# Kernel tuning notes

Measured on AMD Instinct MI355X. Metric: run time of the kernel, lower is better.

## Reference

```python
import jax, jax.numpy as jnp
import numpy as np

NEG = -1e18


def _split_heads(x, h):
    # [B, L, D] -> [B, H, L, D/H]
    b, l, d = x.shape
    return x.reshape(b, l, h, d // h).transpose(0, 2, 1, 3)


def _merge_heads(x):
    # [B, H, L, Dh] -> [B, L, H*Dh]
    b, h, l, dh = x.shape
    return x.transpose(0, 2, 1, 3).reshape(b, l, h * dh)


def _sparse(att, dp_map):
    # att: [B, H, L] per-token scores; dp_map: [B, 2, L] (row, col) tree indices.
    # scatter att[b,h,t] -> S[b, h, dp_map[b,0,t], dp_map[b,1,t]], then symmetrize.
    B, H, L = att.shape
    bi = jnp.arange(B)[:, None, None]          # [B,1,1]
    hi = jnp.arange(H)[None, :, None]          # [1,H,1]
    p0 = dp_map[:, 0, :][:, None, :]           # [B,1,L]
    p1 = dp_map[:, 1, :][:, None, :]           # [B,1,L]
    s = jnp.zeros((B, H, L, L), att.dtype)
    s = s.at[bi, hi, p0, p1].set(att)          # matches torch index_put_ (overwrite)
    return s + jnp.swapaxes(s, 2, 3)


def _reverse(values, dp_map):
    # r[b, j] = values[b, dp_map[b,0,j]] for j >= 1; r[b,0] = 0
    idx = dp_map[:, 0, :]                      # [B, L]
    r = jnp.take_along_axis(values, idx[:, :, None], axis=1)
    return r.at[:, 0, :].set(0.0)


def setup_inputs() -> dict:
    key = jax.random.key(0)
    ks = jax.random.split(key, 16)
    B, L, D, R, H = 16, 384, 768, 768, 12
    inp = {
        "queries":   jax.random.normal(ks[0], (B, L, D), jnp.float32),
        "keys":      jax.random.normal(ks[1], (B, L, D), jnp.float32),
        "values":    jax.random.normal(ks[2], (B, L, D), jnp.float32),
        "relations": jax.random.normal(ks[3], (B, L, R), jnp.float32),
        "dp_map":    jax.random.randint(ks[4], (B, 2, L), 0, L, jnp.int32),
        "mask":      jax.random.bernoulli(ks[5], 0.1, (B, L, L)),
        "rel_mask":  jax.random.bernoulli(ks[6], 0.1, (B, L, 1)),
        "Wq":  jax.random.normal(ks[7],  (D, D), jnp.float32) * 0.02,
        "Wk":  jax.random.normal(ks[8],  (D, D), jnp.float32) * 0.02,
        "Wv":  jax.random.normal(ks[9],  (D, D), jnp.float32) * 0.02,
        "Wo":  jax.random.normal(ks[10], (D, D), jnp.float32) * 0.02,
        "Wge": jax.random.normal(ks[11], (D, R), jnp.float32) * 0.02,
        "Wgr": jax.random.normal(ks[12], (R, R), jnp.float32) * 0.02,
        "Vr":  jax.random.normal(ks[13], (R, 1), jnp.float32) * 0.02,
        "Vg":  jax.random.normal(ks[14], (R, 1), jnp.float32) * 0.02,
    }
    return inp


def reference(queries, keys, values, relations, dp_map, mask, rel_mask,
              Wq, Wk, Wv, Wo, Wge, Wgr, Vr, Vg):
    H = 12
    R = Vg.shape[0]
    Dk = Wq.shape[1]
    scale = (Dk // H) ** -0.5

    # config.is_reverse = True path
    hv = jnp.where(rel_mask, 0.0, _reverse(values, dp_map))       # [B,L,D]
    rel = jnp.where(rel_mask, 0.0, relations)                     # [B,L,R]

    # semantic gated mechanism
    rv_h = _split_heads(rel @ Wgr, H)                             # [B,H,L,R/H]
    hs_h = _split_heads(hv @ Wge, H)
    Vg_h = Vg.reshape(H, R // H, 1)
    g = jnp.tanh(jnp.einsum('bhld,hdo->bhlo', hs_h + rv_h, Vg_h))[..., 0]
    gated = _sparse(g, dp_map)                                    # [B,H,L,L]

    q = _split_heads(queries @ Wq, H) * scale
    k = _split_heads(keys @ Wk, H)
    v = _split_heads(values @ Wv, H)
    rel_h = _split_heads(rel, H)
    Vr_h = Vr.reshape(H, R // H, 1)

    self_logits = jnp.einsum('bhqd,bhkd->bhqk', q, k)             # [B,H,L,L]
    rel_logits = _sparse(jnp.einsum('bhld,hdo->bhlo', rel_h, Vr_h)[..., 0], dp_map)

    m = mask[:, None]                                             # [B,1,L,L]
    self_logits = jnp.where(m, NEG, self_logits)
    rel_logits = jnp.where(m, NEG, rel_logits)

    attention_weights = self_logits.sum(axis=1) / H               # [B,L,L]
    sw = jax.nn.softmax(self_logits, axis=-1)
    rw = jax.nn.softmax(rel_logits, axis=-1)
    w = (1.0 - gated) * sw + gated * rw                           # dropout p=0

    ctx = jnp.einsum('bhqk,bhkd->bhqd', w, v)
    out = _merge_heads(ctx) @ Wo
    return out, attention_weights
```

## Files before the change

kernel.cpp:

```cpp
#include <hip/hip_runtime.h>
#include <math.h>

#define Bn 16
#define Lq 384
#define Hn 12
#define Dm 768
#define DH 64
#define QT2 16
#define NEGV (-1e18f)
#define SPADU 404
#define ECAP 32

typedef __attribute__((ext_vector_type(4))) float f32x4;
typedef __attribute__((ext_vector_type(8))) __bf16 bf16x8;
typedef __attribute__((ext_vector_type(4))) __bf16 bf16x4;
typedef unsigned short ushort_t;
typedef unsigned int uint_t;
typedef unsigned long long ull_t;

__device__ __forceinline__ ushort_t f2b(float f) {
  return __builtin_bit_cast(ushort_t, (__bf16)f);
}
__device__ __forceinline__ float b2f(ushort_t u) {
  return __uint_as_float(((unsigned int)u) << 16);
}
__device__ __forceinline__ bf16x8 cvt8(float4 a, float4 b) {
  bf16x8 r;
  r[0] = (__bf16)a.x; r[1] = (__bf16)a.y; r[2] = (__bf16)a.z; r[3] = (__bf16)a.w;
  r[4] = (__bf16)b.x; r[5] = (__bf16)b.y; r[6] = (__bf16)b.z; r[7] = (__bf16)b.w;
  return r;
}

__global__ __launch_bounds__(256) void k_prep(
    const float* __restrict__ Wge, const float* __restrict__ Wgr,
    const float* __restrict__ Vg,
    float* __restrict__ Age, float* __restrict__ Agr,
    const float* __restrict__ W0, const float* __restrict__ W1,
    const float* __restrict__ W2, const float* __restrict__ W3,
    ushort_t* __restrict__ T0, ushort_t* __restrict__ T1,
    ushort_t* __restrict__ T2, ushort_t* __restrict__ T3,
    const int* __restrict__ dp, int* __restrict__ win,
    const int* __restrict__ mask, ull_t* __restrict__ mbits)
{
  __shared__ float vg[DH];
  __shared__ float t[32][33];
  int blk = blockIdx.x;
  if (blk < 24) {
    int which = blk / Hn;
    int h = blk % Hn;
    const float* Wsrc = which ? Wgr : Wge;
    float* dst = which ? Agr : Age;
    if (threadIdx.x < DH) vg[threadIdx.x] = Vg[h*DH + threadIdx.x];
    __syncthreads();
    for (int d = threadIdx.x; d < Dm; d += 256) {
      const float* wrow = Wsrc + (size_t)d*Dm + h*DH;
      float s = 0.f;
      #pragma unroll 8
      for (int j = 0; j < DH; ++j) s = fmaf(wrow[j], vg[j], s);
      dst[h*Dm + d] = s;
    }
  } else if (blk < 24 + 2304) {
    int b2 = blk - 24;
    int z = b2 / 576, rem = b2 % 576;
    const float* W = (z == 0) ? W0 : (z == 1) ? W1 : (z == 2) ? W2 : W3;
    ushort_t* WT = (z == 0) ? T0 : (z == 1) ? T1 : (z == 2) ? T2 : T3;
    int k0 = (rem / 24)*32, n0 = (rem % 24)*32;
    int tx = threadIdx.x & 31, ty = threadIdx.x >> 5;
    #pragma unroll
    for (int r = 0; r < 4; ++r)
      t[ty + r*8][tx] = W[(size_t)(k0 + ty + r*8)*Dm + n0 + tx];
    __syncthreads();
    #pragma unroll
    for (int r = 0; r < 4; ++r)
      WT[(size_t)(n0 + ty + r*8)*Dm + k0 + tx] = f2b(t[tx][ty + r*8]);
  } else if (blk < 2352) {
    int i = (blk - 2328)*256 + threadIdx.x;
    int b = i / Lq, l = i % Lq;
    int p0 = dp[(size_t)(b*2+0)*Lq + l];
    int p1 = dp[(size_t)(b*2+1)*Lq + l];
    atomicMax(&win[(size_t)b*Lq*Lq + (size_t)p0*Lq + p1], l);
  } else {
    int rr = blk - 2352;
    int lane = threadIdx.x & 63, wave = threadIdx.x >> 6;
    int gi = rr*4 + wave;
    const int* mrow = mask + (size_t)gi*Lq;
    ull_t w0 = __ballot(mrow[lane]        != 0);
    ull_t w1 = __ballot(mrow[lane + 64]   != 0);
    ull_t w2 = __ballot(mrow[lane + 128]  != 0);
    ull_t w3 = __ballot(mrow[lane + 192]  != 0);
    ull_t w4 = __ballot(mrow[lane + 256]  != 0);
    ull_t w5 = __ballot(mrow[lane + 320]  != 0);
    if (lane == 0) {
      ull_t* out = mbits + (size_t)gi*6;
      out[0] = w0; out[1] = w1; out[2] = w2;
      out[3] = w3; out[4] = w4; out[5] = w5;
    }
  }
}

__global__ __launch_bounds__(256) void k_collect(
    const int* __restrict__ win, uint_t* __restrict__ ent,
    int* __restrict__ rowcnt)
{
  __shared__ int tB[32][33];
  int b = blockIdx.z;
  int i0 = blockIdx.x*32, j0 = blockIdx.y*32;
  const int* wb = win + (size_t)b*Lq*Lq;
  int tx = threadIdx.x & 31, ty = threadIdx.x >> 5;
  #pragma unroll
  for (int rr = 0; rr < 4; ++rr) {
    int r = ty + rr*8;
    tB[r][tx] = wb[(size_t)(j0+r)*Lq + i0 + tx];
  }
  __syncthreads();
  #pragma unroll
  for (int rr = 0; rr < 4; ++rr) {
    int ti = ty + rr*8;
    int i = i0 + ti, j = j0 + tx;
    int l1 = wb[(size_t)i*Lq + j];
    int l2 = tB[tx][ti];
    if (l1 >= 0 || l2 >= 0) {
      int slot = atomicAdd(&rowcnt[(size_t)b*Lq + i], 1);
      if (slot < ECAP)
        ent[((size_t)b*Lq + i)*ECAP + slot] =
            (uint_t)j | ((uint_t)(l1 + 1) << 9) | ((uint_t)(l2 + 1) << 19);
    }
  }
}

__global__ __launch_bounds__(256) void k_grlog(
    const float* __restrict__ values, const float* __restrict__ relations,
    const int* __restrict__ dp, const int* __restrict__ rel_mask,
    const float* __restrict__ Age, const float* __restrict__ Agr,
    const float* __restrict__ Vr,
    float* __restrict__ g, float* __restrict__ rlog)
{
  int blk = blockIdx.x;
  int b = blk / (Lq/4), l0 = (blk % (Lq/4))*4;
  int tid = threadIdx.x, lane = tid & 63, wave = tid >> 6;
  __shared__ float relrow[4][Dm], hvrow[4][Dm];
  #pragma unroll
  for (int rr = 0; rr < 4; ++rr) {
    int l = l0 + rr;
    int rm = rel_mask[(size_t)b*Lq + l];
    int idx = dp[(size_t)(b*2)*Lq + l];
    const float* vrow = values + ((size_t)b*Lq + idx)*Dm;
    const float* rrow = relations + ((size_t)b*Lq + l)*Dm;
    for (int d = tid; d < Dm; d += 256) {
      relrow[rr][d] = rm ? 0.f : rrow[d];
      hvrow[rr][d]  = (rm || l == 0) ? 0.f : vrow[d];
    }
  }
  __syncthreads();
  int l = l0 + wave;
  for (int h = 0; h < Hn; ++h) {
    float p = 0.f;
    #pragma unroll
    for (int k = 0; k < Dm/64; ++k) {
      int d = lane + 64*k;
      p = fmaf(hvrow[wave][d], Age[h*Dm + d],
          fmaf(relrow[wave][d], Agr[h*Dm + d], p));
    }
    #pragma unroll
    for (int o = 32; o > 0; o >>= 1) p += __shfl_xor(p, o);
    if (lane == 0) g[((size_t)b*Hn + h)*Lq + l] = tanhf(p);
  }
  if (lane < Hn) {
    float s = 0.f;
    #pragma unroll 8
    for (int j = 0; j < DH; ++j)
      s = fmaf(relrow[wave][lane*DH + j], Vr[lane*DH + j], s);
    rlog[((size_t)b*Hn + lane)*Lq + l] = s;
  }
}

__global__ __launch_bounds__(256) void k_mmqkv(
    const float* __restrict__ Xq, const float* __restrict__ Xk,
    const float* __restrict__ Xv,
    const ushort_t* __restrict__ WqT, const ushort_t* __restrict__ WkT,
    const ushort_t* __restrict__ WvT,
    ushort_t* __restrict__ qbf, ushort_t* __restrict__ kbf,
    ushort_t* __restrict__ vTbf)
{
  __shared__ ushort_t As[64*64];
  __shared__ ushort_t Bs[128*64];

  int z = blockIdx.z;
  const float* A     = (z == 0) ? Xq : (z == 1) ? Xk : Xv;
  const ushort_t* BT = (z == 0) ? WqT : (z == 1) ? WkT : WvT;

  int bm = blockIdx.x;
  int bn = blockIdx.y;
  int m0 = bm*64, n0 = bn*128;

  int t = threadIdx.x;
  int wave = t >> 6, lane = t & 63;
  int wr = wave >> 1, wc = wave & 1;
  int lrow = lane & 15, lkg = lane >> 4;
  int sr = t >> 3, sc8 = t & 7;

  f32x4 acc[2][4];
  #pragma unroll
  for (int i = 0; i < 2; ++i)
    #pragma unroll
    for (int j = 0; j < 4; ++j) acc[i][j] = (f32x4)(0.f);

  for (int k0 = 0; k0 < Dm; k0 += 64) {
    __syncthreads();
    #pragma unroll
    for (int i = 0; i < 2; ++i) {
      int row = sr + i*32;
      const float* ap = A + (size_t)(m0 + row)*Dm + k0 + sc8*8;
      float4 f0 = *(const float4*)ap;
      float4 f1 = *(const float4*)(ap + 4);
      *(bf16x8*)&As[row*64 + (sc8 ^ (row & 7))*8] = cvt8(f0, f1);
    }
    #pragma unroll
    for (int i = 0; i < 4; ++i) {
      int row = sr + i*32;
      uint4 vb = *(const uint4*)(BT + (size_t)(n0 + row)*Dm + k0 + sc8*8);
      *(uint4*)&Bs[row*64 + (sc8 ^ (row & 7))*8] = vb;
    }
    __syncthreads();
    #pragma unroll
    for (int kk = 0; kk < 2; ++kk) {
      bf16x8 aF[2], bF[4];
      int chunk = kk*4 + lkg;
      #pragma unroll
      for (int mi = 0; mi < 2; ++mi) {
        int arow = wr*32 + mi*16 + lrow;
        aF[mi] = *(const bf16x8*)&As[arow*64 + ((chunk ^ (arow & 7)) << 3)];
      }
      #pragma unroll
      for (int ni = 0; ni < 4; ++ni) {
        int brow = wc*64 + ni*16 + lrow;
        bF[ni] = *(const bf16x8*)&Bs[brow*64 + ((chunk ^ (brow & 7)) << 3)];
      }
      #pragma unroll
      for (int mi = 0; mi < 2; ++mi)
        #pragma unroll
        for (int ni = 0; ni < 4; ++ni)
          acc[mi][ni] = __builtin_amdgcn_mfma_f32_16x16x32_bf16(
              aF[mi], bF[ni], acc[mi][ni], 0, 0, 0);
    }
  }

  float alpha = (z == 0) ? 0.125f : 1.f;
  #pragma unroll
  for (int mi = 0; mi < 2; ++mi) {
    #pragma unroll
    for (int ni = 0; ni < 4; ++ni) {
      f32x4 a = acc[mi][ni];
      int rit = wr*32 + mi*16 + 4*lkg;
      int cit = wc*64 + ni*16 + lrow;
      int gcol = n0 + cit;
      if (z < 2) {
        ushort_t* Cb = z ? kbf : qbf;
        int grow = m0 + rit;
        #pragma unroll
        for (int r = 0; r < 4; ++r)
          Cb[(size_t)(grow + r)*Dm + gcol] = f2b(a[r]*alpha);
      } else {
        int b = bm/6;
        int rl = (bm%6)*64 + rit;
        ushort4 u;
        u.x = f2b(a[0]); u.y = f2b(a[1]); u.z = f2b(a[2]); u.w = f2b(a[3]);
        *(ushort4*)&vTbf[((size_t)b*Dm + gcol)*Lq + rl] = u;
      }
    }
  }
}

template<int MODE>
__global__ __launch_bounds__(256) void k_mm64(
    const ushort_t* __restrict__ A, const ushort_t* __restrict__ BT,
    float* __restrict__ Cf, const int* __restrict__ mask, float alpha)
{
  const int K = Dm;
  __shared__ ushort_t As[64*64];
  __shared__ ushort_t Bs[128*64];

  int bm = blockIdx.x, bn = blockIdx.y, b = blockIdx.z;
  const ushort_t* Ab = (MODE == 3) ? A  + (size_t)b*Lq*Dm : A;
  const ushort_t* Bb = (MODE == 3) ? BT + (size_t)b*Lq*Dm : BT;
  int m0 = bm*64, n0 = bn*128;

  int t = threadIdx.x;
  int wave = t >> 6, lane = t & 63;
  int wr = wave >> 1, wc = wave & 1;
  int lrow = lane & 15, lkg = lane >> 4;

  f32x4 acc[2][4];
  #pragma unroll
  for (int i = 0; i < 2; ++i)
    #pragma unroll
    for (int j = 0; j < 4; ++j) acc[i][j] = (f32x4)(0.f);

  int sr = t >> 3, sc8 = t & 7;
  for (int k0 = 0; k0 < K; k0 += 64) {
    __syncthreads();
    #pragma unroll
    for (int i = 0; i < 2; ++i) {
      int row = sr + i*32;
      uint4 va = *(const uint4*)(Ab + (size_t)(m0 + row)*K + k0 + sc8*8);
      int slot = sc8 ^ (row & 7);
      *(uint4*)&As[row*64 + slot*8] = va;
    }
    #pragma unroll
    for (int i = 0; i < 4; ++i) {
      int row = sr + i*32;
      uint4 vb = *(const uint4*)(Bb + (size_t)(n0 + row)*K + k0 + sc8*8);
      int slot = sc8 ^ (row & 7);
      *(uint4*)&Bs[row*64 + slot*8] = vb;
    }
    __syncthreads();
    #pragma unroll
    for (int kk = 0; kk < 2; ++kk) {
      bf16x8 aF[2], bF[4];
      int chunk = kk*4 + lkg;
      #pragma unroll
      for (int mi = 0; mi < 2; ++mi) {
        int arow = wr*32 + mi*16 + lrow;
        aF[mi] = *(const bf16x8*)&As[arow*64 + ((chunk ^ (arow & 7)) << 3)];
      }
      #pragma unroll
      for (int ni = 0; ni < 4; ++ni) {
        int brow = wc*64 + ni*16 + lrow;
        bF[ni] = *(const bf16x8*)&Bs[brow*64 + ((chunk ^ (brow & 7)) << 3)];
      }
      #pragma unroll
      for (int mi = 0; mi < 2; ++mi)
        #pragma unroll
        for (int ni = 0; ni < 4; ++ni)
          acc[mi][ni] = __builtin_amdgcn_mfma_f32_16x16x32_bf16(
              aF[mi], bF[ni], acc[mi][ni], 0, 0, 0);
    }
  }

  #pragma unroll
  for (int mi = 0; mi < 2; ++mi) {
    #pragma unroll
    for (int ni = 0; ni < 4; ++ni) {
      f32x4 a = acc[mi][ni];
      int rit = wr*32 + mi*16 + 4*lkg;
      int cit = wc*64 + ni*16 + lrow;
      if (MODE == 0) {
        int grow = m0 + rit, gcol = n0 + cit;
        #pragma unroll
        for (int r = 0; r < 4; ++r)
          Cf[(size_t)(grow + r)*Dm + gcol] = a[r]*alpha;
      } else {
        int rl = m0 + rit, cl = n0 + cit;
        const int* mb2 = mask + (size_t)b*Lq*Lq;
        float* awb = Cf + (size_t)b*Lq*Lq;
        #pragma unroll
        for (int r = 0; r < 4; ++r) {
          int m = mb2[(size_t)(rl + r)*Lq + cl];
          awb[(size_t)(rl + r)*Lq + cl] = m ? NEGV : a[r]*alpha;
        }
      }
    }
  }
}

__global__ __launch_bounds__(256, 8) void k_attn3(
    const ushort_t* __restrict__ qbf, const ushort_t* __restrict__ kbf,
    const ushort_t* __restrict__ vT,
    const ull_t* __restrict__ mbits, const int* __restrict__ rowcnt,
    const uint_t* __restrict__ ent,
    const float* __restrict__ g, const float* __restrict__ rlog,
    ushort_t* __restrict__ ctxbf)
{
  __shared__ ushort_t S16[QT2][SPADU];
  __shared__ ull_t mb[QT2][6];
  __shared__ float2 rg2[Lq + 1];
  __shared__ uint_t entS[QT2*ECAP];
  __shared__ int cntS[QT2];
  __shared__ float pp[QT2][4];
  __shared__ float sinvS[QT2];

  int bid = blockIdx.x;
  int h  = bid % Hn;
  int qt = (bid / Hn) % (Lq/QT2);
  int b  = bid / (Hn * (Lq/QT2));
  int q0 = qt * QT2;
  int tid = threadIdx.x, lane = tid & 63, wave = tid >> 6;
  int lrow = lane & 15, lkg = lane >> 4;

  const float* gh = g    + ((size_t)b*Hn + h)*Lq;
  const float* rh = rlog + ((size_t)b*Hn + h)*Lq;

  if (tid < QT2*6) {
    int r = tid / 6, u = tid % 6;
    mb[r][u] = mbits[((size_t)b*Lq + q0 + r)*6 + u];
  }
  if (tid == 0) { rg2[0].x = 0.f; rg2[0].y = 0.f; }
  for (int e = tid; e < Lq; e += 256) {
    float2 v2; v2.x = rh[e]; v2.y = gh[e];
    rg2[e + 1] = v2;
  }
  #pragma unroll
  for (int e = tid; e < QT2*ECAP; e += 256)
    entS[e] = ent[((size_t)b*Lq + q0)*ECAP + e];
  if (tid < QT2) {
    int c = rowcnt[(size_t)b*Lq + q0 + tid];
    cntS[tid] = c > ECAP ? ECAP : c;
  }
  __syncthreads();

  {
    const ushort_t* qb = qbf + ((size_t)b*Lq + q0 + lrow)*Dm + h*DH + lkg*8;
    bf16x8 aF0 = *(const bf16x8*)(qb);
    bf16x8 aF1 = *(const bf16x8*)(qb + 32);
    int col0 = wave*96;
    int w0 = col0 >> 6;
    ull_t m0[4], m1[4];
    #pragma unroll
    for (int r = 0; r < 4; ++r) {
      m0[r] = mb[4*lkg + r][w0];
      m1[r] = mb[4*lkg + r][w0 + 1];
    }
    float ps[4] = {0.f, 0.f, 0.f, 0.f};
    const ushort_t* kb = kbf + ((size_t)b*Lq + col0 + lrow)*Dm + h*DH + lkg*8;
    #pragma unroll
    for (int tt = 0; tt < 6; ++tt) {
      int col = col0 + tt*16 + lrow;
      bf16x8 bF0 = *(const bf16x8*)(kb);
      bf16x8 bF1 = *(const bf16x8*)(kb + 32);
      kb += 16*Dm;
      f32x4 z = (f32x4)(0.f);
      z = __builtin_amdgcn_mfma_f32_16x16x32_bf16(aF0, bF0, z, 0, 0, 0);
      z = __builtin_amdgcn_mfma_f32_16x16x32_bf16(aF1, bF1, z, 0, 0, 0);
      bool hi = ((col0 + tt*16) >> 6) != w0;
      int sh = col & 63;
      #pragma unroll
      for (int r = 0; r < 4; ++r) {
        ull_t mw = hi ? m1[r] : m0[r];
        bool mk = (mw >> sh) & 1ull;
        float e = mk ? 0.f : __expf(z[r]);
        ps[r] += e;
        S16[4*lkg + r][col] = f2b(e);
      }
    }
    #pragma unroll
    for (int off = 1; off < 16; off <<= 1)
      #pragma unroll
      for (int r = 0; r < 4; ++r) ps[r] += __shfl_xor(ps[r], off);
    if (lrow == 0) {
      #pragma unroll
      for (int r = 0; r < 4; ++r) pp[4*lkg + r][wave] = ps[r];
    }
  }
  __syncthreads();

  if (tid < QT2) {
    int row = tid;
    float ssum = pp[row][0] + pp[row][1] + pp[row][2] + pp[row][3];
    float si = 1.f / ssum;
    sinvS[row] = si;
    int nun = 384;
    #pragma unroll
    for (int u = 0; u < 6; ++u) nun -= (int)__popcll(mb[row][u]);
    int cnt = cntS[row];
    const uint_t* erow = &entS[row*ECAP];
    float rext = 0.f;
    for (int e = 0; e < cnt; ++e) {
      uint_t en = erow[e];
      int j = en & 511;
      if ((mb[row][j >> 6] >> (j & 63)) & 1ull) continue;
      float rel = rg2[(en >> 9) & 1023].x + rg2[en >> 19].x;
      rext += __expf(rel) - 1.f;
    }
    float sr = ssum / ((float)nun + rext);
    for (int e = 0; e < cnt; ++e) {
      uint_t en = erow[e];
      int j = en & 511;
      if ((mb[row][j >> 6] >> (j & 63)) & 1ull) continue;
      float2 a = rg2[(en >> 9) & 1023];
      float2 c = rg2[en >> 19];
      float er = __expf(a.x + c.x);
      float gvv = a.y + c.y;
      float ev = b2f(S16[row][j]);
      S16[row][j] = f2b((1.f - gvv)*ev + gvv*er*sr);
    }
  }
  __syncthreads();

  {
    int dcol = h*DH + wave*16 + lrow;
    const ushort_t* vb = vT + ((size_t)b*Dm + dcol)*Lq + lkg*8;
    const ushort_t* prow = &S16[lrow][0];
    f32x4 o = (f32x4)(0.f);
    #pragma unroll
    for (int ks = 0; ks < 12; ++ks) {
      bf16x4 lo = *(const bf16x4*)(prow + ks*32 + lkg*8);
      bf16x4 hi = *(const bf16x4*)(prow + ks*32 + lkg*8 + 4);
      bf16x8 pa = __builtin_shufflevector(lo, hi, 0,1,2,3,4,5,6,7);
      bf16x8 bv = *(const bf16x8*)(vb + ks*32);
      o = __builtin_amdgcn_mfma_f32_16x16x32_bf16(pa, bv, o, 0, 0, 0);
    }
    #pragma unroll
    for (int r = 0; r < 4; ++r) {
      float si = sinvS[4*lkg + r];
      ctxbf[((size_t)b*Lq + q0 + 4*lkg + r)*Dm + dcol] = f2b(o[r]*si);
    }
  }
}

extern "C" void kernel_launch(void* const* d_in, const int* in_sizes, int n_in,
                              void* d_out, int out_size, void* d_ws, size_t ws_size,
                              hipStream_t stream) {
  const float* queries   = (const float*)d_in[0];
  const float* keys      = (const float*)d_in[1];
  const float* values    = (const float*)d_in[2];
  const float* relations = (const float*)d_in[3];
  const int*   dp_map    = (const int*)d_in[4];
  const int*   mask      = (const int*)d_in[5];
  const int*   rel_mask  = (const int*)d_in[6];
  const float* Wq  = (const float*)d_in[7];
  const float* Wk  = (const float*)d_in[8];
  const float* Wv  = (const float*)d_in[9];
  const float* Wo  = (const float*)d_in[10];
  const float* Wge = (const float*)d_in[11];
  const float* Wgr = (const float*)d_in[12];
  const float* Vr  = (const float*)d_in[13];
  const float* Vg  = (const float*)d_in[14];

  float* ws = (float*)d_ws;
  const size_t SZ   = (size_t)Bn*Lq*Dm;
  const size_t WINS = (size_t)Bn*Lq*Lq;
  const size_t GSZ  = (size_t)Bn*Hn*Lq;
  const size_t ROWS = (size_t)Bn*Lq;

  int*   win  = (int*)ws;
  float* g    = ws + WINS;
  float* rlog = g + GSZ;
  float* Age  = rlog + GSZ;
  float* Agr  = Age + (size_t)Hn*Dm;
  ull_t* mbits = (ull_t*)(Agr + (size_t)Hn*Dm);
  int*   rowcnt = (int*)(mbits + ROWS*6);
  uint_t* ent  = (uint_t*)(rowcnt + ROWS);
  ushort_t* p0 = (ushort_t*)(ent + ROWS*ECAP);
  ushort_t* qbf  = p0;
  ushort_t* kbf  = p0 + SZ;
  ushort_t* vTbf = p0 + 2*SZ;
  ushort_t* ctxbf= p0 + 3*SZ;
  ushort_t* WqT  = p0 + 4*SZ;
  ushort_t* WkT  = WqT + (size_t)Dm*Dm;
  ushort_t* WvT  = WkT + (size_t)Dm*Dm;
  ushort_t* WoT  = WvT + (size_t)Dm*Dm;

  float* outp = (float*)d_out;
  float* awp  = outp + SZ;

  hipMemsetAsync(win, 0xFF, WINS*sizeof(int), stream);
  hipMemsetAsync(rowcnt, 0, ROWS*sizeof(int), stream);
  k_prep<<<3888, 256, 0, stream>>>(Wge, Wgr, Vg, Age, Agr,
                                   Wq, Wk, Wv, Wo, WqT, WkT, WvT, WoT,
                                   dp_map, win, mask, mbits);
  k_grlog<<<Bn*Lq/4, 256, 0, stream>>>(values, relations, dp_map, rel_mask,
                                       Age, Agr, Vr, g, rlog);
  k_mmqkv<<<dim3(96, 6, 3), 256, 0, stream>>>(queries, keys, values,
                                              WqT, WkT, WvT, qbf, kbf, vTbf);
  k_collect<<<dim3(12, 12, Bn), 256, 0, stream>>>(win, ent, rowcnt);
  k_mm64<3><<<dim3(6, 3, Bn), 256, 0, stream>>>(qbf, kbf, awp, mask, 1.f/12.f);
  k_attn3<<<Bn*(Lq/QT2)*Hn, 256, 0, stream>>>(qbf, kbf, vTbf, mbits, rowcnt,
                                              ent, g, rlog, ctxbf);
  k_mm64<0><<<dim3(96, 6, 1), 256, 0, stream>>>(ctxbf, WoT, outp, nullptr, 1.f);
}
```

Baseline: 195.0 us.

## Merge independent stage kernels into two block-dispatched megakernels

Independent kernels (gate/relation logits, QKV projection, entry collection) are merged into one launch. Attention-weight GEMM and attention are merged into a second launch, each dispatching by block index into device functions that share a fixed shared-memory buffer. This cuts launch count and lets independent work from different stages overlap on the GPU. In exchange, every block reserves the largest shared-memory footprint, and the attention kernel loses its occupancy launch-bound hint, which may reduce residency for attention blocks.

```diff
diff --git a/kernel.cpp b/kernel.cpp
--- a/kernel.cpp
+++ b/kernel.cpp
@@ -30,6 +30,8 @@
   r[4] = (__bf16)b.x; r[5] = (__bf16)b.y; r[6] = (__bf16)b.z; r[7] = (__bf16)b.w;
   return r;
 }
+
+#define SMEM_BYTES 24576
 
 __global__ __launch_bounds__(256) void k_prep(
     const float* __restrict__ Wge, const float* __restrict__ Wgr,
@@ -98,47 +100,17 @@
   }
 }
 
-__global__ __launch_bounds__(256) void k_collect(
-    const int* __restrict__ win, uint_t* __restrict__ ent,
-    int* __restrict__ rowcnt)
-{
-  __shared__ int tB[32][33];
-  int b = blockIdx.z;
-  int i0 = blockIdx.x*32, j0 = blockIdx.y*32;
-  const int* wb = win + (size_t)b*Lq*Lq;
-  int tx = threadIdx.x & 31, ty = threadIdx.x >> 5;
-  #pragma unroll
-  for (int rr = 0; rr < 4; ++rr) {
-    int r = ty + rr*8;
-    tB[r][tx] = wb[(size_t)(j0+r)*Lq + i0 + tx];
-  }
-  __syncthreads();
-  #pragma unroll
-  for (int rr = 0; rr < 4; ++rr) {
-    int ti = ty + rr*8;
-    int i = i0 + ti, j = j0 + tx;
-    int l1 = wb[(size_t)i*Lq + j];
-    int l2 = tB[tx][ti];
-    if (l1 >= 0 || l2 >= 0) {
-      int slot = atomicAdd(&rowcnt[(size_t)b*Lq + i], 1);
-      if (slot < ECAP)
-        ent[((size_t)b*Lq + i)*ECAP + slot] =
-            (uint_t)j | ((uint_t)(l1 + 1) << 9) | ((uint_t)(l2 + 1) << 19);
-    }
-  }
-}
-
-__global__ __launch_bounds__(256) void k_grlog(
+
+__device__ void dev_grlog(char* sm, int blk,
     const float* __restrict__ values, const float* __restrict__ relations,
     const int* __restrict__ dp, const int* __restrict__ rel_mask,
     const float* __restrict__ Age, const float* __restrict__ Agr,
-    const float* __restrict__ Vr,
-    float* __restrict__ g, float* __restrict__ rlog)
-{
-  int blk = blockIdx.x;
+    const float* __restrict__ Vr, float* __restrict__ g, float* __restrict__ rlog)
+{
+  float (*relrow)[Dm] = (float(*)[Dm])sm;
+  float (*hvrow)[Dm]  = (float(*)[Dm])(sm + 4*Dm*sizeof(float));
   int b = blk / (Lq/4), l0 = (blk % (Lq/4))*4;
   int tid = threadIdx.x, lane = tid & 63, wave = tid >> 6;
-  __shared__ float relrow[4][Dm], hvrow[4][Dm];
   #pragma unroll
   for (int rr = 0; rr < 4; ++rr) {
     int l = l0 + rr;
@@ -174,7 +146,7 @@
   }
 }
 
-__global__ __launch_bounds__(256) void k_mmqkv(
+__device__ void dev_mmqkv(char* sm, int bm, int bn, int z,
     const float* __restrict__ Xq, const float* __restrict__ Xk,
     const float* __restrict__ Xv,
     const ushort_t* __restrict__ WqT, const ushort_t* __restrict__ WkT,
@@ -182,17 +154,11 @@
     ushort_t* __restrict__ qbf, ushort_t* __restrict__ kbf,
     ushort_t* __restrict__ vTbf)
 {
-  __shared__ ushort_t As[64*64];
-  __shared__ ushort_t Bs[128*64];
-
-  int z = blockIdx.z;
+  ushort_t* As = (ushort_t*)sm;
+  ushort_t* Bs = (ushort_t*)(sm + 8192);
   const float* A     = (z == 0) ? Xq : (z == 1) ? Xk : Xv;
   const ushort_t* BT = (z == 0) ? WqT : (z == 1) ? WkT : WvT;
-
-  int bm = blockIdx.x;
-  int bn = blockIdx.y;
   int m0 = bm*64, n0 = bn*128;
-
   int t = threadIdx.x;
   int wave = t >> 6, lane = t & 63;
   int wr = wave >> 1, wc = wave & 1;
@@ -253,7 +219,7 @@
       f32x4 a = acc[mi][ni];
       int rit = wr*32 + mi*16 + 4*lkg;
       int cit = wc*64 + ni*16 + lrow;
-      int gcol = n0 + cit;
+      int gcol = bn*128 + cit;
       if (z < 2) {
         ushort_t* Cb = z ? kbf : qbf;
         int grow = m0 + rit;
@@ -271,24 +237,49 @@
   }
 }
 
-template<int MODE>
-__global__ __launch_bounds__(256) void k_mm64(
+__device__ void dev_collect(char* sm, int i0b, int j0b, int b,
+    const int* __restrict__ win, uint_t* __restrict__ ent,
+    int* __restrict__ rowcnt)
+{
+  int (*tB)[33] = (int(*)[33])sm;
+  int i0 = i0b*32, j0 = j0b*32;
+  const int* wb = win + (size_t)b*Lq*Lq;
+  int tx = threadIdx.x & 31, ty = threadIdx.x >> 5;
+  #pragma unroll
+  for (int rr = 0; rr < 4; ++rr) {
+    int r = ty + rr*8;
+    tB[r][tx] = wb[(size_t)(j0+r)*Lq + i0 + tx];
+  }
+  __syncthreads();
+  #pragma unroll
+  for (int rr = 0; rr < 4; ++rr) {
+    int ti = ty + rr*8;
+    int i = i0 + ti, j = j0 + tx;
+    int l1 = wb[(size_t)i*Lq + j];
+    int l2 = tB[tx][ti];
+    if (l1 >= 0 || l2 >= 0) {
+      int slot = atomicAdd(&rowcnt[(size_t)b*Lq + i], 1);
+      if (slot < ECAP)
+        ent[((size_t)b*Lq + i)*ECAP + slot] =
+            (uint_t)j | ((uint_t)(l1 + 1) << 9) | ((uint_t)(l2 + 1) << 19);
+    }
+  }
+}
+
+__device__ void dev_aw(char* sm, int bm, int bn, int b,
     const ushort_t* __restrict__ A, const ushort_t* __restrict__ BT,
     float* __restrict__ Cf, const int* __restrict__ mask, float alpha)
 {
-  const int K = Dm;
-  __shared__ ushort_t As[64*64];
-  __shared__ ushort_t Bs[128*64];
-
-  int bm = blockIdx.x, bn = blockIdx.y, b = blockIdx.z;
-  const ushort_t* Ab = (MODE == 3) ? A  + (size_t)b*Lq*Dm : A;
-  const ushort_t* Bb = (MODE == 3) ? BT + (size_t)b*Lq*Dm : BT;
+  ushort_t* As = (ushort_t*)sm;
+  ushort_t* Bs = (ushort_t*)(sm + 8192);
+  const ushort_t* Ab = A  + (size_t)b*Lq*Dm;
+  const ushort_t* Bb = BT + (size_t)b*Lq*Dm;
   int m0 = bm*64, n0 = bn*128;
-
   int t = threadIdx.x;
   int wave = t >> 6, lane = t & 63;
   int wr = wave >> 1, wc = wave & 1;
   int lrow = lane & 15, lkg = lane >> 4;
+  int sr = t >> 3, sc8 = t & 7;
 
   f32x4 acc[2][4];
   #pragma unroll
@@ -296,22 +287,19 @@
     #pragma unroll
     for (int j = 0; j < 4; ++j) acc[i][j] = (f32x4)(0.f);
 
-  int sr = t >> 3, sc8 = t & 7;
-  for (int k0 = 0; k0 < K; k0 += 64) {
+  for (int k0 = 0; k0 < Dm; k0 += 64) {
     __syncthreads();
     #pragma unroll
     for (int i = 0; i < 2; ++i) {
       int row = sr + i*32;
-      uint4 va = *(const uint4*)(Ab + (size_t)(m0 + row)*K + k0 + sc8*8);
-      int slot = sc8 ^ (row & 7);
-      *(uint4*)&As[row*64 + slot*8] = va;
+      uint4 va = *(const uint4*)(Ab + (size_t)(m0 + row)*Dm + k0 + sc8*8);
+      *(uint4*)&As[row*64 + (sc8 ^ (row & 7))*8] = va;
     }
     #pragma unroll
     for (int i = 0; i < 4; ++i) {
       int row = sr + i*32;
-      uint4 vb = *(const uint4*)(Bb + (size_t)(n0 + row)*K + k0 + sc8*8);
-      int slot = sc8 ^ (row & 7);
-      *(uint4*)&Bs[row*64 + slot*8] = vb;
+      uint4 vb = *(const uint4*)(Bb + (size_t)(n0 + row)*Dm + k0 + sc8*8);
+      *(uint4*)&Bs[row*64 + (sc8 ^ (row & 7))*8] = vb;
     }
     __syncthreads();
     #pragma unroll
@@ -344,26 +332,29 @@
       f32x4 a = acc[mi][ni];
       int rit = wr*32 + mi*16 + 4*lkg;
       int cit = wc*64 + ni*16 + lrow;
-      if (MODE == 0) {
-        int grow = m0 + rit, gcol = n0 + cit;
-        #pragma unroll
-        for (int r = 0; r < 4; ++r)
-          Cf[(size_t)(grow + r)*Dm + gcol] = a[r]*alpha;
-      } else {
-        int rl = m0 + rit, cl = n0 + cit;
-        const int* mb2 = mask + (size_t)b*Lq*Lq;
-        float* awb = Cf + (size_t)b*Lq*Lq;
-        #pragma unroll
-        for (int r = 0; r < 4; ++r) {
-          int m = mb2[(size_t)(rl + r)*Lq + cl];
-          awb[(size_t)(rl + r)*Lq + cl] = m ? NEGV : a[r]*alpha;
-        }
-      }
-    }
-  }
-}
-
-__global__ __launch_bounds__(256, 8) void k_attn3(
+      int rl = m0 + rit, cl = n0 + cit;
+      const int* mb2 = mask + (size_t)b*Lq*Lq;
+      float* awb = Cf + (size_t)b*Lq*Lq;
+      #pragma unroll
+      for (int r = 0; r < 4; ++r) {
+        int m = mb2[(size_t)(rl + r)*Lq + cl];
+        awb[(size_t)(rl + r)*Lq + cl] = m ? NEGV : a[r]*alpha;
+      }
+    }
+  }
+}
+
+struct AttnS {
+  ushort_t S16[QT2][SPADU];
+  ull_t mb[QT2][6];
+  float2 rg2[Lq + 1];
+  uint_t entS[QT2*ECAP];
+  int cntS[QT2];
+  float pp[QT2][4];
+  float sinvS[QT2];
+};
+
+__device__ void dev_attn3(char* sm, int bid,
     const ushort_t* __restrict__ qbf, const ushort_t* __restrict__ kbf,
     const ushort_t* __restrict__ vT,
     const ull_t* __restrict__ mbits, const int* __restrict__ rowcnt,
@@ -371,15 +362,7 @@
     const float* __restrict__ g, const float* __restrict__ rlog,
     ushort_t* __restrict__ ctxbf)
 {
-  __shared__ ushort_t S16[QT2][SPADU];
-  __shared__ ull_t mb[QT2][6];
-  __shared__ float2 rg2[Lq + 1];
-  __shared__ uint_t entS[QT2*ECAP];
-  __shared__ int cntS[QT2];
-  __shared__ float pp[QT2][4];
-  __shared__ float sinvS[QT2];
-
-  int bid = blockIdx.x;
+  AttnS* S = (AttnS*)sm;
   int h  = bid % Hn;
   int qt = (bid / Hn) % (Lq/QT2);
   int b  = bid / (Hn * (Lq/QT2));
@@ -392,19 +375,19 @@
 
   if (tid < QT2*6) {
     int r = tid / 6, u = tid % 6;
-    mb[r][u] = mbits[((size_t)b*Lq + q0 + r)*6 + u];
-  }
-  if (tid == 0) { rg2[0].x = 0.f; rg2[0].y = 0.f; }
+    S->mb[r][u] = mbits[((size_t)b*Lq + q0 + r)*6 + u];
+  }
+  if (tid == 0) { S->rg2[0].x = 0.f; S->rg2[0].y = 0.f; }
   for (int e = tid; e < Lq; e += 256) {
     float2 v2; v2.x = rh[e]; v2.y = gh[e];
-    rg2[e + 1] = v2;
+    S->rg2[e + 1] = v2;
   }
   #pragma unroll
   for (int e = tid; e < QT2*ECAP; e += 256)
-    entS[e] = ent[((size_t)b*Lq + q0)*ECAP + e];
+    S->entS[e] = ent[((size_t)b*Lq + q0)*ECAP + e];
   if (tid < QT2) {
     int c = rowcnt[(size_t)b*Lq + q0 + tid];
-    cntS[tid] = c > ECAP ? ECAP : c;
+    S->cntS[tid] = c > ECAP ? ECAP : c;
   }
   __syncthreads();
 
@@ -417,8 +400,8 @@
     ull_t m0[4], m1[4];
     #pragma unroll
     for (int r = 0; r < 4; ++r) {
-      m0[r] = mb[4*lkg + r][w0];
-      m1[r] = mb[4*lkg + r][w0 + 1];
+      m0[r] = S->mb[4*lkg + r][w0];
+      m1[r] = S->mb[4*lkg + r][w0 + 1];
     }
     float ps[4] = {0.f, 0.f, 0.f, 0.f};
     const ushort_t* kb = kbf + ((size_t)b*Lq + col0 + lrow)*Dm + h*DH + lkg*8;
@@ -439,7 +422,7 @@
         bool mk = (mw >> sh) & 1ull;
         float e = mk ? 0.f : __expf(z[r]);
         ps[r] += e;
-        S16[4*lkg + r][col] = f2b(e);
+        S->S16[4*lkg + r][col] = f2b(e);
       }
     }
     #pragma unroll
@@ -448,40 +431,40 @@
       for (int r = 0; r < 4; ++r) ps[r] += __shfl_xor(ps[r], off);
     if (lrow == 0) {
       #pragma unroll
-      for (int r = 0; r < 4; ++r) pp[4*lkg + r][wave] = ps[r];
+      for (int r = 0; r < 4; ++r) S->pp[4*lkg + r][wave] = ps[r];
     }
   }
   __syncthreads();
 
   if (tid < QT2) {
     int row = tid;
-    float ssum = pp[row][0] + pp[row][1] + pp[row][2] + pp[row][3];
+    float ssum = S->pp[row][0] + S->pp[row][1] + S->pp[row][2] + S->pp[row][3];
     float si = 1.f / ssum;
-    sinvS[row] = si;
+    S->sinvS[row] = si;
     int nun = 384;
     #pragma unroll
-    for (int u = 0; u < 6; ++u) nun -= (int)__popcll(mb[row][u]);
-    int cnt = cntS[row];
-    const uint_t* erow = &entS[row*ECAP];
+    for (int u = 0; u < 6; ++u) nun -= (int)__popcll(S->mb[row][u]);
+    int cnt = S->cntS[row];
+    const uint_t* erow = &S->entS[row*ECAP];
     float rext = 0.f;
     for (int e = 0; e < cnt; ++e) {
       uint_t en = erow[e];
       int j = en & 511;
-      if ((mb[row][j >> 6] >> (j & 63)) & 1ull) continue;
-      float rel = rg2[(en >> 9) & 1023].x + rg2[en >> 19].x;
+      if ((S->mb[row][j >> 6] >> (j & 63)) & 1ull) continue;
+      float rel = S->rg2[(en >> 9) & 1023].x + S->rg2[en >> 19].x;
       rext += __expf(rel) - 1.f;
     }
     float sr = ssum / ((float)nun + rext);
     for (int e = 0; e < cnt; ++e) {
       uint_t en = erow[e];
       int j = en & 511;
-      if ((mb[row][j >> 6] >> (j & 63)) & 1ull) continue;
-      float2 a = rg2[(en >> 9) & 1023];
-      float2 c = rg2[en >> 19];
+      if ((S->mb[row][j >> 6] >> (j & 63)) & 1ull) continue;
+      float2 a = S->rg2[(en >> 9) & 1023];
+      float2 c = S->rg2[en >> 19];
       float er = __expf(a.x + c.x);
       float gvv = a.y + c.y;
-      float ev = b2f(S16[row][j]);
-      S16[row][j] = f2b((1.f - gvv)*ev + gvv*er*sr);
+      float ev = b2f(S->S16[row][j]);
+      S->S16[row][j] = f2b((1.f - gvv)*ev + gvv*er*sr);
     }
   }
   __syncthreads();
@@ -489,7 +472,7 @@
   {
     int dcol = h*DH + wave*16 + lrow;
     const ushort_t* vb = vT + ((size_t)b*Dm + dcol)*Lq + lkg*8;
-    const ushort_t* prow = &S16[lrow][0];
+    const ushort_t* prow = &S->S16[lrow][0];
     f32x4 o = (f32x4)(0.f);
     #pragma unroll
     for (int ks = 0; ks < 12; ++ks) {
@@ -501,8 +484,126 @@
     }
     #pragma unroll
     for (int r = 0; r < 4; ++r) {
-      float si = sinvS[4*lkg + r];
+      float si = S->sinvS[4*lkg + r];
       ctxbf[((size_t)b*Lq + q0 + 4*lkg + r)*Dm + dcol] = f2b(o[r]*si);
+    }
+  }
+}
+
+
+__global__ __launch_bounds__(256) void k_mega1(
+    const float* __restrict__ values, const float* __restrict__ relations,
+    const int* __restrict__ dp, const int* __restrict__ rel_mask,
+    const float* __restrict__ Age, const float* __restrict__ Agr,
+    const float* __restrict__ Vr, float* __restrict__ g, float* __restrict__ rlog,
+    const float* __restrict__ Xq, const float* __restrict__ Xk,
+    const float* __restrict__ Xv,
+    const ushort_t* __restrict__ WqT, const ushort_t* __restrict__ WkT,
+    const ushort_t* __restrict__ WvT,
+    ushort_t* __restrict__ qbf, ushort_t* __restrict__ kbf,
+    ushort_t* __restrict__ vTbf,
+    const int* __restrict__ win, uint_t* __restrict__ ent,
+    int* __restrict__ rowcnt)
+{
+  __shared__ __align__(16) char sm[SMEM_BYTES];
+  int blk = blockIdx.x;
+  if (blk < 1536) {
+    dev_grlog(sm, blk, values, relations, dp, rel_mask, Age, Agr, Vr, g, rlog);
+  } else if (blk < 3264) {
+    int t = blk - 1536;
+    dev_mmqkv(sm, t % 96, (t/96) % 6, t/576, Xq, Xk, Xv, WqT, WkT, WvT,
+              qbf, kbf, vTbf);
+  } else {
+    int t = blk - 3264;
+    dev_collect(sm, t % 12, (t/12) % 12, t/144, win, ent, rowcnt);
+  }
+}
+
+__global__ __launch_bounds__(256) void k_mega2(
+    const ushort_t* __restrict__ qbf, const ushort_t* __restrict__ kbf,
+    const ushort_t* __restrict__ vTbf,
+    const ull_t* __restrict__ mbits, const int* __restrict__ rowcnt,
+    const uint_t* __restrict__ ent,
+    const float* __restrict__ g, const float* __restrict__ rlog,
+    ushort_t* __restrict__ ctxbf,
+    const int* __restrict__ mask, float* __restrict__ awp)
+{
+  __shared__ __align__(16) char sm[SMEM_BYTES];
+  int blk = blockIdx.x;
+  if (blk < 288) {
+    dev_aw(sm, blk % 6, (blk/6) % 3, blk/18, qbf, kbf, awp, mask, 1.f/12.f);
+  } else {
+    dev_attn3(sm, blk - 288, qbf, kbf, vTbf, mbits, rowcnt, ent, g, rlog, ctxbf);
+  }
+}
+
+__global__ __launch_bounds__(256) void k_mmout(
+    const ushort_t* __restrict__ A, const ushort_t* __restrict__ BT,
+    float* __restrict__ Cf)
+{
+  __shared__ ushort_t As[64*64];
+  __shared__ ushort_t Bs[128*64];
+  int m0 = blockIdx.x*64, n0 = blockIdx.y*128;
+  int t = threadIdx.x;
+  int wave = t >> 6, lane = t & 63;
+  int wr = wave >> 1, wc = wave & 1;
+  int lrow = lane & 15, lkg = lane >> 4;
+  int sr = t >> 3, sc8 = t & 7;
+
+  f32x4 acc[2][4];
+  #pragma unroll
+  for (int i = 0; i < 2; ++i)
+    #pragma unroll
+    for (int j = 0; j < 4; ++j) acc[i][j] = (f32x4)(0.f);
+
+  for (int k0 = 0; k0 < Dm; k0 += 64) {
+    __syncthreads();
+    #pragma unroll
+    for (int i = 0; i < 2; ++i) {
+      int row = sr + i*32;
+      uint4 va = *(const uint4*)(A + (size_t)(m0 + row)*Dm + k0 + sc8*8);
+      *(uint4*)&As[row*64 + (sc8 ^ (row & 7))*8] = va;
+    }
+    #pragma unroll
+    for (int i = 0; i < 4; ++i) {
+      int row = sr + i*32;
+      uint4 vb = *(const uint4*)(BT + (size_t)(n0 + row)*Dm + k0 + sc8*8);
+      *(uint4*)&Bs[row*64 + (sc8 ^ (row & 7))*8] = vb;
+    }
+    __syncthreads();
+    #pragma unroll
+    for (int kk = 0; kk < 2; ++kk) {
+      bf16x8 aF[2], bF[4];
+      int chunk = kk*4 + lkg;
+      #pragma unroll
+      for (int mi = 0; mi < 2; ++mi) {
+        int arow = wr*32 + mi*16 + lrow;
+        aF[mi] = *(const bf16x8*)&As[arow*64 + ((chunk ^ (arow & 7)) << 3)];
+      }
+      #pragma unroll
+      for (int ni = 0; ni < 4; ++ni) {
+        int brow = wc*64 + ni*16 + lrow;
+        bF[ni] = *(const bf16x8*)&Bs[brow*64 + ((chunk ^ (brow & 7)) << 3)];
+      }
+      #pragma unroll
+      for (int mi = 0; mi < 2; ++mi)
+        #pragma unroll
+        for (int ni = 0; ni < 4; ++ni)
+          acc[mi][ni] = __builtin_amdgcn_mfma_f32_16x16x32_bf16(
+              aF[mi], bF[ni], acc[mi][ni], 0, 0, 0);
+    }
+  }
+
+  #pragma unroll
+  for (int mi = 0; mi < 2; ++mi) {
+    #pragma unroll
+    for (int ni = 0; ni < 4; ++ni) {
+      f32x4 a = acc[mi][ni];
+      int grow = m0 + wr*32 + mi*16 + 4*lkg;
+      int gcol = n0 + wc*64 + ni*16 + lrow;
+      #pragma unroll
+      for (int r = 0; r < 4; ++r)
+        Cf[(size_t)(grow + r)*Dm + gcol] = a[r];
     }
   }
 }
@@ -558,13 +659,11 @@
   k_prep<<<3888, 256, 0, stream>>>(Wge, Wgr, Vg, Age, Agr,
                                    Wq, Wk, Wv, Wo, WqT, WkT, WvT, WoT,
                                    dp_map, win, mask, mbits);
-  k_grlog<<<Bn*Lq/4, 256, 0, stream>>>(values, relations, dp_map, rel_mask,
-                                       Age, Agr, Vr, g, rlog);
-  k_mmqkv<<<dim3(96, 6, 3), 256, 0, stream>>>(queries, keys, values,
-                                              WqT, WkT, WvT, qbf, kbf, vTbf);
-  k_collect<<<dim3(12, 12, Bn), 256, 0, stream>>>(win, ent, rowcnt);
-  k_mm64<3><<<dim3(6, 3, Bn), 256, 0, stream>>>(qbf, kbf, awp, mask, 1.f/12.f);
-  k_attn3<<<Bn*(Lq/QT2)*Hn, 256, 0, stream>>>(qbf, kbf, vTbf, mbits, rowcnt,
-                                              ent, g, rlog, ctxbf);
-  k_mm64<0><<<dim3(96, 6, 1), 256, 0, stream>>>(ctxbf, WoT, outp, nullptr, 1.f);
-}
+  k_mega1<<<5568, 256, 0, stream>>>(values, relations, dp_map, rel_mask,
+                                    Age, Agr, Vr, g, rlog,
+                                    queries, keys, values, WqT, WkT, WvT,
+                                    qbf, kbf, vTbf, win, ent, rowcnt);
+  k_mega2<<<4896, 256, 0, stream>>>(qbf, kbf, vTbf, mbits, rowcnt, ent,
+                                    g, rlog, ctxbf, mask, awp);
+  k_mmout<<<dim3(96, 6), 256, 0, stream>>>(ctxbf, WoT, outp);
+}
```

Measured after the change: 180.6 us. 7.4% less time.
